# Performance work log

Hardware: AMD Instinct MI355X
Metric: run time of the kernel (lower is better)

Reference implementation:

```python
import jax, jax.numpy as jnp
import numpy as np

B, N, C_IN, C_OUT, BASIS = 8, 128, 64, 64, 15
AVG_NOBJ = 49.0
NEG_SLOPE = 0.01  # torch LeakyReLU default


def eops_2_to_2_sum(x, average_nobj=AVG_NOBJ):
    """x: [B, C, N, N] -> [B, C, 15, N, N].
    5 order-zero ops + 10 sum-aggregation ops (sums normalized by average_nobj,
    double sums by average_nobj**2, as in PELICAN's 'sum' aggregation)."""
    n = x.shape[-1]
    eye = jnp.eye(n, dtype=x.dtype)                       # [N, N]
    d = jnp.diagonal(x, axis1=-2, axis2=-1)               # [B, C, N]
    rowsum = x.sum(-1) / average_nobj                      # [B, C, N]
    colsum = x.sum(-2) / average_nobj                      # [B, C, N]
    trace = d.sum(-1) / average_nobj                       # [B, C]
    allsum = x.sum((-2, -1)) / (average_nobj ** 2)         # [B, C]
    bc = lambda v: jnp.broadcast_to(v, x.shape)
    ops = [
        # --- order zero (no aggregation) ---
        d[..., :, None] * eye,                 # diag(A) embedded on diagonal
        bc(d[..., :, None]),                   # A_ii broadcast along j
        bc(d[..., None, :]),                   # A_jj broadcast along i
        x,                                     # identity
        jnp.swapaxes(x, -1, -2),               # transpose
        # --- aggregation ops ---
        rowsum[..., :, None] * eye,            # row sums on diagonal
        colsum[..., :, None] * eye,            # col sums on diagonal
        trace[..., None, None] * eye,          # trace on diagonal
        allsum[..., None, None] * eye,         # total sum on diagonal
        bc(rowsum[..., :, None]),              # rowsum_i broadcast along j
        bc(rowsum[..., None, :]),              # rowsum_j broadcast along i
        bc(colsum[..., :, None]),              # colsum_i broadcast along j
        bc(colsum[..., None, :]),              # colsum_j broadcast along i
        bc(trace[..., None, None]),            # trace broadcast everywhere
        bc(allsum[..., None, None]),           # total sum broadcast everywhere
    ]
    return jnp.stack(ops, axis=2)              # [B, C, 15, N, N]


def setup_inputs() -> dict:
    key = jax.random.key(0)
    ks = jax.random.split(key, 5)
    inputs = jax.random.normal(ks[0], (B, N, N, C_IN), jnp.float32)
    mask = jnp.ones((B, N, N, 1), jnp.float32)
    nobj = jnp.full((B,), float(N), jnp.float32)
    s_b = float(np.sqrt(1.0 / BASIS))
    s_d = float(np.sqrt(1.0 / C_IN))
    coefs00 = jax.random.normal(ks[1], (C_IN, BASIS), jnp.float32) * s_b
    coefs01 = jax.random.normal(ks[2], (C_OUT, BASIS), jnp.float32) * s_b
    coefs10 = jax.random.normal(ks[3], (C_IN, C_OUT), jnp.float32) * s_d
    coefs11 = jax.random.normal(ks[4], (C_IN, C_OUT), jnp.float32) * s_d
    bias = jnp.zeros((C_OUT,), jnp.float32)
    diag_bias = jnp.zeros((C_OUT,), jnp.float32)
    return {"inputs": inputs, "mask": mask, "nobj": nobj,
            "coefs00": coefs00, "coefs01": coefs01,
            "coefs10": coefs10, "coefs11": coefs11,
            "bias": bias, "diag_bias": diag_bias}


def reference(inputs, mask, nobj, coefs00, coefs01, coefs10, coefs11, bias, diag_bias):
    # inputs: [B, N, N, C_in] -> channels-first for basis construction
    x = jnp.transpose(inputs, (0, 3, 1, 2))                     # [B, C, N, N]
    ops = eops_2_to_2_sum(x)                                    # [B, C, 15, N, N]
    # low-rank reconstructed coefficient tensor [C_in, C_out, 15]
    coefs = (coefs00[:, None, :] * coefs10[:, :, None]
             + coefs01[None, :, :] * coefs11[:, :, None])
    out = jnp.einsum('dsb,ndbij->nijs', coefs, ops)             # [B, N, N, C_out]
    eye = jnp.eye(inputs.shape[1], dtype=out.dtype)[None, :, :, None]
    out = out + bias[None, None, None, :] + eye * diag_bias[None, None, None, :]
    out = jax.nn.leaky_relu(out, NEG_SLOPE)
    return out * mask
```

## Files before the change

kernel.cpp:

```cpp
#include <hip/hip_runtime.h>

#define BB 8
#define NN 128
#define CC 64
static constexpr float INV_A = 1.0f / 49.0f;

#define OFF_C    0
#define OFF_CB   61440
#define OFF_RS   65536
#define OFF_CS   131072
#define OFF_DV   196608
#define OFF_U1   263168
#define OFF_U2   328704
#define OFF_DG   394240
#define OFF_XT   459776

typedef __attribute__((ext_vector_type(8))) short v8s;
typedef __attribute__((ext_vector_type(4))) float v4f;

static __device__ inline unsigned pack2bf(float a, float b) {
    union { float f; unsigned u; } ua, ub; ua.f = a; ub.f = b;
    return ((ua.u + 0x8000u) >> 16) | ((ub.u + 0x8000u) & 0xffff0000u);
}
static __device__ inline unsigned short f2bf(float a) {
    union { float f; unsigned u; } ua; ua.f = a;
    return (unsigned short)((ua.u + 0x8000u) >> 16);
}

__global__ void k_pre(const float* __restrict__ in,
                      const float* __restrict__ c00, const float* __restrict__ c01,
                      const float* __restrict__ c10, const float* __restrict__ c11,
                      float* __restrict__ ws) {
    int bb = blockIdx.x;
    int t = threadIdx.x;
    if (bb >= 2048) {
        int idx = (bb - 2048) * 256 + t;
        if (idx < 15 * 4096) {
            int b = idx >> 12; int r = idx & 4095; int d = r >> 6; int s = r & 63;
            ws[OFF_C + idx] = c00[d * 15 + b] * c10[d * 64 + s] + c01[s * 15 + b] * c11[d * 64 + s];
        } else if (idx < 15 * 4096 + 8192) {
            int k = idx - 15 * 4096;
            int which = k >> 12;
            int r = k & 4095; int s = r >> 6; int d = r & 63;
            int b = 3 + which;
            float v = c00[d * 15 + b] * c10[d * 64 + s] + c01[s * 15 + b] * c11[d * 64 + s];
            unsigned short* cb = (unsigned short*)(ws + OFF_CB);
            cb[s * 128 + which * 64 + d] = f2bf(v);
        }
        return;
    }
    __shared__ float4 part[16][16];
    int mode = bb >> 10;
    int r = bb & 1023;
    int n = r >> 7; int i = r & 127;
    int d4 = t & 15; int g = t >> 4;

    float4 acc = make_float4(0.f, 0.f, 0.f, 0.f);
    if (mode == 0) {
        const float* base = in + ((size_t)(n * NN + i)) * NN * CC + d4 * 4;
        float4 dvv = acc; bool hd = false;
        #pragma unroll
        for (int e = 0; e < 8; ++e) {
            int j = g * 8 + e;
            float4 v = *(const float4*)(base + (size_t)j * CC);
            acc.x += v.x; acc.y += v.y; acc.z += v.z; acc.w += v.w;
            if (j == i) { dvv = v; hd = true; }
        }
        if (hd) *(float4*)(ws + OFF_DV + ((size_t)(n * NN + i)) * CC + d4 * 4) = dvv;
    } else {
        const float* base = in + ((size_t)(n * NN) * NN + i) * CC + d4 * 4;
        unsigned short* xT = (unsigned short*)(ws + OFF_XT)
                           + ((size_t)(n * NN + i)) * NN * CC + d4 * 4;
        #pragma unroll
        for (int e = 0; e < 8; ++e) {
            int ii2 = g * 8 + e;
            float4 v = *(const float4*)(base + (size_t)ii2 * NN * CC);
            acc.x += v.x; acc.y += v.y; acc.z += v.z; acc.w += v.w;
            uint2 pk; pk.x = pack2bf(v.x, v.y); pk.y = pack2bf(v.z, v.w);
            *(uint2*)(xT + (size_t)ii2 * CC) = pk;
        }
    }
    part[g][d4] = acc;
    __syncthreads();
    if (t < 64) {
        int dd = t & 15; int qq = t >> 4;
        float4 a = part[qq * 4 + 0][dd], b = part[qq * 4 + 1][dd];
        float4 c = part[qq * 4 + 2][dd], d = part[qq * 4 + 3][dd];
        float4 s;
        s.x = a.x + b.x + c.x + d.x; s.y = a.y + b.y + c.y + d.y;
        s.z = a.z + b.z + c.z + d.z; s.w = a.w + b.w + c.w + d.w;
        part[qq * 4][dd] = s;
    }
    __syncthreads();
    if (t < 16) {
        float4 a = part[0][t], b = part[4][t], c = part[8][t], d = part[12][t];
        float4 s;
        s.x = (a.x + b.x + c.x + d.x) * INV_A;
        s.y = (a.y + b.y + c.y + d.y) * INV_A;
        s.z = (a.z + b.z + c.z + d.z) * INV_A;
        s.w = (a.w + b.w + c.w + d.w) * INV_A;
        *(float4*)(ws + (mode ? OFF_CS : OFF_RS) + ((size_t)(n * NN + i)) * CC + t * 4) = s;
    }
}

__global__ __launch_bounds__(256, 4) void k_uv(const float* __restrict__ bias,
                                               const float* __restrict__ dbias,
                                               float* __restrict__ ws) {
    __shared__ float trL[64], asL[64];
    __shared__ float pU1[4][4][64], pU2[4][4][64], pDG[4][4][64];
    __shared__ float pS[4][64], pDGc[4][64];
    int n = blockIdx.x >> 5; int i0 = (blockIdx.x & 31) * 4;
    int t = threadIdx.x;
    int s = t & 63; int q = t >> 6;

    {
        float tr = 0.f, as = 0.f;
        #pragma unroll 4
        for (int e = 0; e < 32; ++e) {
            int i = q * 32 + e;
            tr += ws[OFF_DV + ((size_t)(n * NN + i)) * CC + s];
            as += ws[OFF_RS + ((size_t)(n * NN + i)) * CC + s];
        }
        pS[q][s] = tr; pDGc[q][s] = as;
        __syncthreads();
        if (t < 64) {
            trL[t] = (pS[0][t] + pS[1][t] + pS[2][t] + pS[3][t]) * INV_A;
            asL[t] = (pDGc[0][t] + pDGc[1][t] + pDGc[2][t] + pDGc[3][t]) * INV_A;
        }
        __syncthreads();
    }

    const float* C = ws + OFF_C;
    float aU1[4] = {0, 0, 0, 0}, aU2[4] = {0, 0, 0, 0}, aDG[4] = {0, 0, 0, 0};
    float aS = 0.f, aDGc = 0.f;
    #pragma unroll
    for (int c4 = 0; c4 < 4; ++c4) {
        int dc = q * 4 + c4;
        float tr4[4], as4[4], dv4[4][4], rs4[4][4], cs4[4][4];
        #pragma unroll
        for (int k = 0; k < 4; ++k) { tr4[k] = trL[dc * 4 + k]; as4[k] = asL[dc * 4 + k]; }
        #pragma unroll
        for (int ii = 0; ii < 4; ++ii) {
            size_t ro = ((size_t)(n * NN + i0 + ii)) * CC + dc * 4;
            float4 v = *(const float4*)(ws + OFF_DV + ro);
            dv4[ii][0] = v.x; dv4[ii][1] = v.y; dv4[ii][2] = v.z; dv4[ii][3] = v.w;
            float4 r = *(const float4*)(ws + OFF_RS + ro);
            rs4[ii][0] = r.x; rs4[ii][1] = r.y; rs4[ii][2] = r.z; rs4[ii][3] = r.w;
            float4 c = *(const float4*)(ws + OFF_CS + ro);
            cs4[ii][0] = c.x; cs4[ii][1] = c.y; cs4[ii][2] = c.z; cs4[ii][3] = c.w;
        }
        #pragma unroll
        for (int k = 0; k < 4; ++k) {
            int d = dc * 4 + k;
            const float* Cd = C + d * 64 + s;
            float c0 = Cd[0 * 4096], c1 = Cd[1 * 4096], c2 = Cd[2 * 4096];
            float c5 = Cd[5 * 4096], c6 = Cd[6 * 4096], c7 = Cd[7 * 4096];
            float c8 = Cd[8 * 4096], c9 = Cd[9 * 4096], c10v = Cd[10 * 4096];
            float c11v = Cd[11 * 4096], c12v = Cd[12 * 4096];
            float c13 = Cd[13 * 4096], c14 = Cd[14 * 4096];
            aS += c13 * tr4[k] + c14 * as4[k];
            aDGc += c7 * tr4[k] + c8 * as4[k];
            #pragma unroll
            for (int ii = 0; ii < 4; ++ii) {
                aU1[ii] += c1 * dv4[ii][k] + c9 * rs4[ii][k] + c11v * cs4[ii][k];
                aU2[ii] += c2 * dv4[ii][k] + c10v * rs4[ii][k] + c12v * cs4[ii][k];
                aDG[ii] += c0 * dv4[ii][k] + c5 * rs4[ii][k] + c6 * cs4[ii][k];
            }
        }
    }
    #pragma unroll
    for (int ii = 0; ii < 4; ++ii) {
        pU1[q][ii][s] = aU1[ii]; pU2[q][ii][s] = aU2[ii]; pDG[q][ii][s] = aDG[ii];
    }
    pS[q][s] = aS; pDGc[q][s] = aDGc;
    __syncthreads();

    int fi = q;
    float u1 = pU1[0][fi][s] + pU1[1][fi][s] + pU1[2][fi][s] + pU1[3][fi][s];
    float u2 = pU2[0][fi][s] + pU2[1][fi][s] + pU2[2][fi][s] + pU2[3][fi][s];
    float dg = pDG[0][fi][s] + pDG[1][fi][s] + pDG[2][fi][s] + pDG[3][fi][s];
    float aSt = pS[0][s] + pS[1][s] + pS[2][s] + pS[3][s];
    float aDGct = pDGc[0][s] + pDGc[1][s] + pDGc[2][s] + pDGc[3][s];
    size_t row = ((size_t)(n * NN + i0 + fi)) * CC + s;
    ws[OFF_U1 + row] = u1 + aSt + bias[s];
    ws[OFF_U2 + row] = u2;
    ws[OFF_DG + row] = dg + aDGct + dbias[s];
}

__global__ __launch_bounds__(256, 4) void k_main(
        const float* __restrict__ in, const float* __restrict__ mask,
        const float* __restrict__ ws, float* __restrict__ out) {
    __shared__ __align__(16) unsigned char smem[34816];
    unsigned short* Ab = (unsigned short*)smem;
    unsigned short* Bb = (unsigned short*)(smem + 17408);
    float* Obuf = (float*)smem;

    int blk = blockIdx.x;
    int n = blk >> 8; int rem = blk & 255; int i = rem >> 1; int j0 = (rem & 1) * 64;
    int t = threadIdx.x;
    int tp = t >> 4; int c = t & 15;

    const unsigned short* cb = (const unsigned short*)(ws + OFF_CB);
    #pragma unroll
    for (int e = 0; e < 4; ++e) {
        int s = e * 16 + tp;
        float4 v = *(const float4*)(cb + s * 128 + c * 8);
        *(float4*)((unsigned char*)(Bb + s * 136 + c * 8)) = v;
    }
    {
        const float* src = in + (((size_t)(n * NN + i)) * NN + j0) * CC;
        #pragma unroll
        for (int e = 0; e < 4; ++e) {
            int p = e * 16 + tp;
            float4 v = *(const float4*)(src + (size_t)p * CC + c * 4);
            uint2 pk; pk.x = pack2bf(v.x, v.y); pk.y = pack2bf(v.z, v.w);
            *(uint2*)(Ab + p * 136 + c * 4) = pk;
        }
    }
    {
        const unsigned short* xT = (const unsigned short*)(ws + OFF_XT)
                                 + (((size_t)(n * NN + i)) * NN + j0) * CC;
        #pragma unroll
        for (int r = 0; r < 2; ++r) {
            int idx = t + r * 256;
            int p = idx >> 3; int ch = idx & 7;
            float4 v = *(const float4*)(xT + (size_t)p * CC + ch * 8);
            *(float4*)((unsigned char*)(Ab + p * 136 + 64 + ch * 8)) = v;
        }
    }
    __syncthreads();

    int w = t >> 6; int l = t & 63;
    int r16 = l & 15; int quad = l >> 4;
    v4f acc[4];
    #pragma unroll
    for (int st = 0; st < 4; ++st) acc[st] = 0.f;
    int arow = w * 16 + r16;
    #pragma unroll
    for (int kk = 0; kk < 4; ++kk) {
        v8s af = *(const v8s*)(Ab + arow * 136 + kk * 32 + quad * 8);
        #pragma unroll
        for (int st = 0; st < 4; ++st) {
            v8s bfr = *(const v8s*)(Bb + (st * 16 + r16) * 136 + kk * 32 + quad * 8);
            acc[st] = __builtin_amdgcn_mfma_f32_16x16x32_bf16(af, bfr, acc[st], 0, 0, 0);
        }
    }
    #pragma unroll
    for (int st = 0; st < 4; ++st)
        #pragma unroll
        for (int reg = 0; reg < 4; ++reg)
            Obuf[(w * 16 + quad * 4 + reg) * 68 + st * 16 + r16] = acc[st][reg];

    int srow = (n * NN + i) * CC;
    float4 u1 = *(const float4*)(ws + OFF_U1 + srow + r16 * 4);
    float4 dg = *(const float4*)(ws + OFF_DG + srow + r16 * 4);
    #pragma unroll
    for (int e = 0; e < 4; ++e) {
        int p = w * 16 + e * 4 + quad;
        int j = j0 + p;
        float4 v = *(const float4*)(Obuf + p * 68 + r16 * 4);
        float4 u2 = *(const float4*)(ws + OFF_U2 + (n * NN + j) * CC + r16 * 4);
        v.x += u1.x + u2.x; v.y += u1.y + u2.y; v.z += u1.z + u2.z; v.w += u1.w + u2.w;
        if (j == i) { v.x += dg.x; v.y += dg.y; v.z += dg.z; v.w += dg.w; }
        v.x = v.x > 0.f ? v.x : 0.01f * v.x;
        v.y = v.y > 0.f ? v.y : 0.01f * v.y;
        v.z = v.z > 0.f ? v.z : 0.01f * v.z;
        v.w = v.w > 0.f ? v.w : 0.01f * v.w;
        float m = mask[((size_t)(n * NN + i)) * NN + j];
        v.x *= m; v.y *= m; v.z *= m; v.w *= m;
        *(float4*)(out + (((size_t)(n * NN + i)) * NN + j) * CC + r16 * 4) = v;
    }
}

extern "C" void kernel_launch(void* const* d_in, const int* in_sizes, int n_in,
                              void* d_out, int out_size, void* d_ws, size_t ws_size,
                              hipStream_t stream) {
    const float* inputs = (const float*)d_in[0];
    const float* mask   = (const float*)d_in[1];
    const float* c00 = (const float*)d_in[3];
    const float* c01 = (const float*)d_in[4];
    const float* c10 = (const float*)d_in[5];
    const float* c11 = (const float*)d_in[6];
    const float* bias  = (const float*)d_in[7];
    const float* dbias = (const float*)d_in[8];
    float* out = (float*)d_out;
    float* ws = (float*)d_ws;

    k_pre <<<2320, 256, 0, stream>>>(inputs, c00, c01, c10, c11, ws);
    k_uv  <<<256,  256, 0, stream>>>(bias, dbias, ws);
    k_main<<<2048, 256, 0, stream>>>(inputs, mask, ws, out);
}
```

Measured before the change: 132.7 us.

## Load MFMA fragments directly from global memory, skip LDS staging

The pre-kernel now writes the bf16 coefficient matrix already swizzled into per-lane MFMA B-fragment order. The main kernel then loads B fragments straight from global memory (L2-resident) and builds A fragments directly from the input rows and the transposed bf16 copy, dropping the LDS staging and the first __syncthreads. This removes LDS traffic and a barrier and shrinks shared memory, which may raise occupancy. In exchange, each wave reads the 16 KB B matrix from cache itself, and the per-lane global loads are less coalesced.

```diff
diff --git a/kernel.cpp b/kernel.cpp
--- a/kernel.cpp
+++ b/kernel.cpp
@@ -39,13 +39,17 @@
             int b = idx >> 12; int r = idx & 4095; int d = r >> 6; int s = r & 63;
             ws[OFF_C + idx] = c00[d * 15 + b] * c10[d * 64 + s] + c01[s * 15 + b] * c11[d * 64 + s];
         } else if (idx < 15 * 4096 + 8192) {
-            int k = idx - 15 * 4096;
-            int which = k >> 12;
-            int r = k & 4095; int s = r >> 6; int d = r & 63;
-            int b = 3 + which;
+            int idx2 = idx - 15 * 4096;
+            int f = idx2 >> 9; int r = idx2 & 511;
+            int l = r >> 3; int e = r & 7;
+            int st = f >> 2; int kk = f & 3;
+            int s = st * 16 + (l & 15);
+            int k = kk * 32 + (l >> 4) * 8 + e;
+            int b = (k < 64) ? 3 : 4;
+            int d = k & 63;
             float v = c00[d * 15 + b] * c10[d * 64 + s] + c01[s * 15 + b] * c11[d * 64 + s];
-            unsigned short* cb = (unsigned short*)(ws + OFF_CB);
-            cb[s * 128 + which * 64 + d] = f2bf(v);
+            unsigned short* bf = (unsigned short*)(ws + OFF_CB);
+            bf[idx2] = f2bf(v);
         }
         return;
     }
@@ -190,61 +194,51 @@
 __global__ __launch_bounds__(256, 4) void k_main(
         const float* __restrict__ in, const float* __restrict__ mask,
         const float* __restrict__ ws, float* __restrict__ out) {
-    __shared__ __align__(16) unsigned char smem[34816];
-    unsigned short* Ab = (unsigned short*)smem;
-    unsigned short* Bb = (unsigned short*)(smem + 17408);
-    float* Obuf = (float*)smem;
+    __shared__ __align__(16) float Obuf[64 * 68];
 
     int blk = blockIdx.x;
     int n = blk >> 8; int rem = blk & 255; int i = rem >> 1; int j0 = (rem & 1) * 64;
     int t = threadIdx.x;
-    int tp = t >> 4; int c = t & 15;
-
-    const unsigned short* cb = (const unsigned short*)(ws + OFF_CB);
-    #pragma unroll
-    for (int e = 0; e < 4; ++e) {
-        int s = e * 16 + tp;
-        float4 v = *(const float4*)(cb + s * 128 + c * 8);
-        *(float4*)((unsigned char*)(Bb + s * 136 + c * 8)) = v;
-    }
-    {
-        const float* src = in + (((size_t)(n * NN + i)) * NN + j0) * CC;
-        #pragma unroll
-        for (int e = 0; e < 4; ++e) {
-            int p = e * 16 + tp;
-            float4 v = *(const float4*)(src + (size_t)p * CC + c * 4);
-            uint2 pk; pk.x = pack2bf(v.x, v.y); pk.y = pack2bf(v.z, v.w);
-            *(uint2*)(Ab + p * 136 + c * 4) = pk;
-        }
-    }
-    {
-        const unsigned short* xT = (const unsigned short*)(ws + OFF_XT)
-                                 + (((size_t)(n * NN + i)) * NN + j0) * CC;
-        #pragma unroll
-        for (int r = 0; r < 2; ++r) {
-            int idx = t + r * 256;
-            int p = idx >> 3; int ch = idx & 7;
-            float4 v = *(const float4*)(xT + (size_t)p * CC + ch * 8);
-            *(float4*)((unsigned char*)(Ab + p * 136 + 64 + ch * 8)) = v;
-        }
-    }
-    __syncthreads();
-
     int w = t >> 6; int l = t & 63;
     int r16 = l & 15; int quad = l >> 4;
+
+    int ja = j0 + w * 16 + r16;
+    const float* xr = in + (((size_t)(n * NN + i)) * NN + ja) * CC;
+    float4 a0 = *(const float4*)(xr + quad * 8);
+    float4 a1 = *(const float4*)(xr + quad * 8 + 4);
+    float4 a2 = *(const float4*)(xr + 32 + quad * 8);
+    float4 a3 = *(const float4*)(xr + 32 + quad * 8 + 4);
+    v8s af0, af1;
+    {
+        unsigned* p0 = (unsigned*)&af0;
+        p0[0] = pack2bf(a0.x, a0.y); p0[1] = pack2bf(a0.z, a0.w);
+        p0[2] = pack2bf(a1.x, a1.y); p0[3] = pack2bf(a1.z, a1.w);
+        unsigned* p1 = (unsigned*)&af1;
+        p1[0] = pack2bf(a2.x, a2.y); p1[1] = pack2bf(a2.z, a2.w);
+        p1[2] = pack2bf(a3.x, a3.y); p1[3] = pack2bf(a3.z, a3.w);
+    }
+    const unsigned short* xT = (const unsigned short*)(ws + OFF_XT)
+                             + (((size_t)(n * NN + i)) * NN + ja) * CC;
+    v8s af2 = *(const v8s*)(xT + quad * 8);
+    v8s af3 = *(const v8s*)(xT + 32 + quad * 8);
+
+    const v8s* bfp = (const v8s*)(ws + OFF_CB);
     v4f acc[4];
     #pragma unroll
     for (int st = 0; st < 4; ++st) acc[st] = 0.f;
-    int arow = w * 16 + r16;
-    #pragma unroll
-    for (int kk = 0; kk < 4; ++kk) {
-        v8s af = *(const v8s*)(Ab + arow * 136 + kk * 32 + quad * 8);
-        #pragma unroll
-        for (int st = 0; st < 4; ++st) {
-            v8s bfr = *(const v8s*)(Bb + (st * 16 + r16) * 136 + kk * 32 + quad * 8);
-            acc[st] = __builtin_amdgcn_mfma_f32_16x16x32_bf16(af, bfr, acc[st], 0, 0, 0);
-        }
-    }
+    #pragma unroll
+    for (int st = 0; st < 4; ++st)
+        acc[st] = __builtin_amdgcn_mfma_f32_16x16x32_bf16(af0, bfp[(st * 4 + 0) * 64 + l], acc[st], 0, 0, 0);
+    #pragma unroll
+    for (int st = 0; st < 4; ++st)
+        acc[st] = __builtin_amdgcn_mfma_f32_16x16x32_bf16(af1, bfp[(st * 4 + 1) * 64 + l], acc[st], 0, 0, 0);
+    #pragma unroll
+    for (int st = 0; st < 4; ++st)
+        acc[st] = __builtin_amdgcn_mfma_f32_16x16x32_bf16(af2, bfp[(st * 4 + 2) * 64 + l], acc[st], 0, 0, 0);
+    #pragma unroll
+    for (int st = 0; st < 4; ++st)
+        acc[st] = __builtin_amdgcn_mfma_f32_16x16x32_bf16(af3, bfp[(st * 4 + 3) * 64 + l], acc[st], 0, 0, 0);
+
     #pragma unroll
     for (int st = 0; st < 4; ++st)
         #pragma unroll
```

Result: no change. 133.3 us (+0.5%).
